# Kernel optimization log

Measured on AMD Instinct MI355X. Metric: run time of the kernel, lower is better.

The kernel has to match this reference:

```python
import jax, jax.numpy as jnp
import numpy as np

B = 16384
LEN_VOCAB = 2048
IPD_VOCAB = 2048
EBDIN = 32


def setup_inputs() -> dict:
    key = jax.random.key(0)
    ks = jax.random.split(key, 11)
    return {
        "x": jax.random.randint(ks[0], (B, 1, 2), 0, LEN_VOCAB, dtype=jnp.int64)
        if jax.config.jax_enable_x64 else jax.random.randint(ks[0], (B, 1, 2), 0, LEN_VOCAB),
        "lenebdLUT": jax.random.normal(ks[1], (LEN_VOCAB, EBDIN), jnp.float32),
        "ipdebdLUT": jax.random.normal(ks[2], (IPD_VOCAB, EBDIN), jnp.float32),
        "S1": jax.random.normal(ks[3], (15, 2, 15), jnp.float32),
        "H1": jax.random.normal(ks[4], (45, 4096), jnp.float32),
        "T1": jax.random.normal(ks[5], (15, 15), jnp.float32),
        "LUT1": jax.random.normal(ks[6], (5, 4096, 32), jnp.float32),
        "S2": jax.random.normal(ks[7], (1, 2, 15), jnp.float32),
        "H2": jax.random.normal(ks[8], (15, 16), jnp.float32),
        "T2": jax.random.normal(ks[9], (1, 15), jnp.float32),
        "LUT2": jax.random.normal(ks[10], (1, 16, 32), jnp.float32),
    }


def _forward(x, lenebdLUT, ipdebdLUT, S1, H1, T1, LUT1, S2, H2, T2, LUT2):
    batch = x.shape[0]
    # embedding lookups, summed: [B,1,32] -> flatten to [B,32] (seq==1)
    e = (lenebdLUT[x[:, :, 0]] + ipdebdLUT[x[:, :, 1]]).reshape(-1, EBDIN)
    ebd = e
    # ---- newMM on first 30 features ----
    a = jnp.einsum('bcd,cdk->bck', e[:, :30].reshape(-1, 15, 2), S1)  # [B,15,15]
    a = a - T1 - 1e-4
    t = jnp.tanh(a)
    a = jax.lax.stop_gradient(jnp.sign(a) - t) + t  # straight-through sign
    a = a.reshape(-1, 5, 45)
    scores1 = jnp.einsum('bcd,dk->bck', a, H1)       # [B,5,4096]
    idx1 = jnp.argmax(scores1, axis=-1)              # [B,5]
    # one_hot(argmax) @ LUT == per-codebook gather
    x1 = LUT1[jnp.arange(5)[None, :], idx1]          # [B,5,32]
    # ---- MM_final on last 2 features ----
    b = jnp.einsum('bcd,cdk->bck', e[:, 30:32].reshape(-1, 1, 2), S2)  # [B,1,15]
    b = b - T2
    b = jnp.where(b == 0, jnp.float32(-1.0), jnp.sign(b))  # x[x==0]=-1; sign(x)
    scores2 = jnp.einsum('bcd,dk->bck', b, H2)       # [B,1,16]
    idx2 = jnp.argmax(scores2, axis=-1)              # [B,1]
    x2 = LUT2[jnp.arange(1)[None, :], idx2]          # [B,1,32]
    x2 = jnp.sum(x2, axis=1).reshape(batch, 1, 32)
    reconstruct = jnp.concatenate([x1, x2], axis=1).sum(axis=1)  # [B,32]
    return reconstruct, ebd


def reference(x, lenebdLUT, ipdebdLUT, S1, H1, T1, LUT1, S2, H2, T2, LUT2):
    return _forward(x, lenebdLUT, ipdebdLUT, S1, H1, T1, LUT1, S2, H2, T2, LUT2)
```

## Files before the change

### kernel.cpp

```cpp
#include <hip/hip_runtime.h>

#define B_TOT 16384
#define NPAIR (B_TOT*5)
#define NPT32 (NPAIR/32)
#define NKG   8
#define KTPG  16
#define KTB   9216

#define PREP_BLKS 288
#define SIGN_BLKS 320
#define EMBD_BLKS 64

typedef __attribute__((ext_vector_type(8))) short bf16x8;
typedef __attribute__((ext_vector_type(16))) float f32x16;

struct alignas(8) us4 { unsigned short x, y, z, w; };

__device__ inline unsigned short f2bf(float f) {
    unsigned u = __builtin_bit_cast(unsigned, f);
    unsigned r = u + 0x7fffu + ((u >> 16) & 1u);
    return (unsigned short)(r >> 16);
}
__device__ inline float bf2f(unsigned short b) {
    unsigned u = ((unsigned)b) << 16;
    return __builtin_bit_cast(float, u);
}
__device__ inline float max3f(float a, float b, float c) {
    return fmaxf(fmaxf(a, b), c);
}

__global__ __launch_bounds__(256) void kfront(
    const int* __restrict__ x,
    const float* __restrict__ lenLUT, const float* __restrict__ ipdLUT,
    const float* __restrict__ S1, const float* __restrict__ H1,
    const float* __restrict__ T1,
    const float* __restrict__ S2, const float* __restrict__ H2,
    const float* __restrict__ T2, const float* __restrict__ LUT2,
    float* __restrict__ out, float* __restrict__ p2vec,
    unsigned short* __restrict__ Abuf, unsigned short* __restrict__ Bbuf) {
    const int bid = blockIdx.x;
    const int tid = threadIdx.x;

    if (bid < PREP_BLKS) {
        int blk = bid * 4 + (tid >> 6);
        int kt = blk / 9, rem = blk - kt*9;
        int s = rem / 3, q = rem - s*3;
        int l = tid & 63;
        int h = l >> 5;
        int row = kt*32 + (l & 31);
        unsigned short o[8];
#pragma unroll
        for (int j = 0; j < 8; ++j) {
            int d = 16*s + 4*h + ((j < 4) ? j : (j + 4));
            float v = (d < 45) ? H1[(size_t)d*4096 + row] : 0.f;
            unsigned short bb = 0;
            for (int qq = 0; qq <= q; ++qq) { bb = f2bf(v); v -= bf2f(bb); }
            o[j] = bb;
        }
        unsigned short* dst = Abuf + (size_t)blk*512 + l*8;
        *(us4*)(dst)     = us4{o[0], o[1], o[2], o[3]};
        *(us4*)(dst + 4) = us4{o[4], o[5], o[6], o[7]};
        return;
    }

    if (bid < PREP_BLKS + SIGN_BLKS) {
        int p = (bid - PREP_BLKS) * 256 + tid;
        int b = p / 5;
        int c = p - b * 5;
        int x0 = x[2*b], x1 = x[2*b+1];
        float e[6];
        const float2* l2 = (const float2*)(lenLUT + (size_t)x0*32 + 6*c);
        const float2* i2 = (const float2*)(ipdLUT + (size_t)x1*32 + 6*c);
#pragma unroll
        for (int t = 0; t < 3; ++t) {
            float2 a = l2[t], d = i2[t];
            e[2*t]   = a.x + d.x;
            e[2*t+1] = a.y + d.y;
        }
        unsigned short sg[48];
#pragma unroll
        for (int t = 0; t < 3; ++t) {
            int c15 = 3*c + t;
#pragma unroll
            for (int k = 0; k < 15; ++k) {
                float a = e[2*t] * S1[(2*c15)*15 + k] + e[2*t+1] * S1[(2*c15+1)*15 + k];
                a = a - T1[c15*15 + k];
                a = a - 1e-4f;
                sg[t*15+k] = (a > 0.f) ? (unsigned short)0x3F80u
                           : ((a < 0.f) ? (unsigned short)0xBF80u : (unsigned short)0);
            }
        }
        sg[45] = 0; sg[46] = 0; sg[47] = 0;
        int P = p >> 5, col = p & 31;
        unsigned short* base = Bbuf + (size_t)P*1536;
#pragma unroll
        for (int s = 0; s < 3; ++s) {
            unsigned short* blk = base + s*512;
            *(us4*)(blk + col*8)          = us4{sg[16*s+0],  sg[16*s+1],  sg[16*s+2],  sg[16*s+3]};
            *(us4*)(blk + col*8 + 4)      = us4{sg[16*s+8],  sg[16*s+9],  sg[16*s+10], sg[16*s+11]};
            *(us4*)(blk + (col+32)*8)     = us4{sg[16*s+4],  sg[16*s+5],  sg[16*s+6],  sg[16*s+7]};
            *(us4*)(blk + (col+32)*8 + 4) = us4{sg[16*s+12], sg[16*s+13], sg[16*s+14], sg[16*s+15]};
        }
        return;
    }

    {
        int b = (bid - PREP_BLKS - SIGN_BLKS) * 256 + tid;
        if (b >= B_TOT) return;
        int x0 = x[2*b], x1 = x[2*b+1];
        const float4* l4 = (const float4*)(lenLUT + (size_t)x0*32);
        const float4* i4 = (const float4*)(ipdLUT + (size_t)x1*32);
        float4* o4 = (float4*)(out + (size_t)B_TOT*32 + (size_t)b*32);
        float e30 = 0.f, e31 = 0.f;
#pragma unroll
        for (int j = 0; j < 8; ++j) {
            float4 a = l4[j], c = i4[j];
            float4 sv; sv.x=a.x+c.x; sv.y=a.y+c.y; sv.z=a.z+c.z; sv.w=a.w+c.w;
            o4[j] = sv;
            if (j == 7) { e30 = sv.z; e31 = sv.w; }
        }
        float sb[15];
#pragma unroll
        for (int k = 0; k < 15; ++k) {
            float bb = e30 * S2[k] + e31 * S2[15 + k];
            bb = bb - T2[k];
            sb[k] = (bb > 0.f) ? 1.f : -1.f;
        }
        float best = -3.4e38f; int bi = 0;
#pragma unroll
        for (int k2 = 0; k2 < 16; ++k2) {
            float sc = 0.f;
#pragma unroll
            for (int d = 0; d < 15; ++d) sc = fmaf(sb[d], H2[d*16 + k2], sc);
            if (sc > best) { best = sc; bi = k2; }
        }
        const float4* lr = (const float4*)(LUT2 + (size_t)bi*32);
        float4* pv = (float4*)(p2vec + (size_t)b*32);
#pragma unroll
        for (int j = 0; j < 8; ++j) pv[j] = lr[j];
    }
}

__global__ __launch_bounds__(256, 3) void k2m(
    const unsigned short* __restrict__ Abuf,
    const unsigned short* __restrict__ Bbuf,
    float* __restrict__ pval, int* __restrict__ pidx) {
    const int bid = blockIdx.x;
    const int kg = bid & 7;
    const int pg = bid >> 3;
    const int tid = threadIdx.x;
    const int w = tid >> 6, l = tid & 63;
    const int pt0 = pg*8 + w*2;

    __shared__ __align__(16) char lds[2][KTB];

    bf16x8 Bf[2][3];
#pragma unroll
    for (int i = 0; i < 2; ++i)
#pragma unroll
        for (int s = 0; s < 3; ++s)
            Bf[i][s] = *(const bf16x8*)(Bbuf + ((size_t)(pt0+i)*3 + s)*512 + l*8);

    float bv16[2][16];
    float V[2] = {-3.4e38f, -3.4e38f};
    int bkt[2] = {0, 0};
#pragma unroll
    for (int i = 0; i < 2; ++i)
#pragma unroll
        for (int r = 0; r < 16; ++r) bv16[i][r] = -3.4e38f;

    const char* Asrc = (const char*)Abuf + (size_t)kg*KTPG*KTB;

#pragma unroll
    for (int r = 0; r < 3; ++r) {
        int idx = tid + r*256;
        if (idx < KTB/16)
            __builtin_amdgcn_global_load_lds(
                (const __attribute__((address_space(1))) unsigned int*)(Asrc + (size_t)idx*16),
                (__attribute__((address_space(3))) unsigned int*)(&lds[0][idx*16]),
                16, 0, 0);
    }
    __syncthreads();

    f32x16 zf;
#pragma unroll
    for (int r = 0; r < 16; ++r) zf[r] = 0.f;

    for (int ktl = 0; ktl < 16; ++ktl) {
        const int cur = ktl & 1;
        if (ktl < 15) {
            const char* src = Asrc + (size_t)(ktl+1)*KTB;
#pragma unroll
            for (int r = 0; r < 3; ++r) {
                int idx = tid + r*256;
                if (idx < KTB/16)
                    __builtin_amdgcn_global_load_lds(
                        (const __attribute__((address_space(1))) unsigned int*)(src + (size_t)idx*16),
                        (__attribute__((address_space(3))) unsigned int*)(&lds[cur^1][idx*16]),
                        16, 0, 0);
            }
        }
        {
            const char* ab = &lds[cur][l*16];
            bf16x8 A[9];
#pragma unroll
            for (int f = 0; f < 9; ++f)
                A[f] = *(const bf16x8*)(ab + f*1024);

            f32x16 acc0, acc1;
            acc0 = __builtin_amdgcn_mfma_f32_32x32x16_bf16(A[0], Bf[0][0], zf, 0, 0, 0);
            acc1 = __builtin_amdgcn_mfma_f32_32x32x16_bf16(A[0], Bf[1][0], zf, 0, 0, 0);
#pragma unroll
            for (int s = 0; s < 3; ++s)
#pragma unroll
                for (int q = 0; q < 3; ++q) {
                    if (s == 0 && q == 0) continue;
                    const int f = s*3 + q;
                    acc0 = __builtin_amdgcn_mfma_f32_32x32x16_bf16(A[f], Bf[0][s], acc0, 0, 0, 0);
                    acc1 = __builtin_amdgcn_mfma_f32_32x32x16_bf16(A[f], Bf[1][s], acc1, 0, 0, 0);
                }
#pragma unroll
            for (int i = 0; i < 2; ++i) {
                const f32x16& a = (i == 0) ? acc0 : acc1;
                float m0 = max3f(a[0],  a[1],  a[2]);
                float m1 = max3f(a[3],  a[4],  a[5]);
                float m2 = max3f(a[6],  a[7],  a[8]);
                float m3 = max3f(a[9],  a[10], a[11]);
                float m4 = max3f(a[12], a[13], a[14]);
                float m5 = max3f(m0, m1, a[15]);
                float m6 = max3f(m2, m3, m4);
                float t  = fmaxf(m5, m6);
                bkt[i] = (t > V[i]) ? ktl : bkt[i];
                V[i] = fmaxf(V[i], t);
#pragma unroll
                for (int r = 0; r < 16; ++r)
                    bv16[i][r] = fmaxf(bv16[i][r], a[r]);
            }
        }
        __syncthreads();
    }

    const int h = l >> 5;
#pragma unroll
    for (int i = 0; i < 2; ++i) {
        int rb = 0;
#pragma unroll
        for (int r = 15; r >= 0; --r)
            rb = (bv16[i][r] == V[i]) ? r : rb;
        int kk = kg*512 + bkt[i]*32 + (rb & 3) + ((rb >> 2) << 3) + (h << 2);
        float v = V[i];
        float ov = __shfl_xor(v, 32);
        int   ok = __shfl_xor(kk, 32);
        if (ov > v || (ov == v && ok < kk)) { v = ov; kk = ok; }
        if (l < 32) {
            int pair = (pt0 + i)*32 + l;
            pval[(size_t)pair*NKG + kg] = v;
            pidx[(size_t)pair*NKG + kg] = kk;
        }
    }
}

__global__ __launch_bounds__(256) void k3_final(
    const float* __restrict__ pval, const int* __restrict__ pidx,
    const float* __restrict__ LUT1, const float* __restrict__ p2vec,
    float* __restrict__ out) {
    int t = blockIdx.x * 256 + threadIdx.x;
    int b = t >> 3, j = t & 7;
    if (b >= B_TOT) return;
    float4 r = ((const float4*)(p2vec + (size_t)b*32))[j];
#pragma unroll
    for (int c = 0; c < 5; ++c) {
        size_t pair = (size_t)b*5 + c;
        const float4* pv4 = (const float4*)(pval + pair*NKG);
        const int4*   pi4 = (const int4*)(pidx + pair*NKG);
        float4 v0 = pv4[0], v1 = pv4[1];
        int4   i0 = pi4[0], i1 = pi4[1];
        float vv[8] = {v0.x, v0.y, v0.z, v0.w, v1.x, v1.y, v1.z, v1.w};
        int   ii[8] = {i0.x, i0.y, i0.z, i0.w, i1.x, i1.y, i1.z, i1.w};
        float bvv = vv[0]; int bk = ii[0];
#pragma unroll
        for (int q = 1; q < 8; ++q) {
            if (vv[q] > bvv) { bvv = vv[q]; bk = ii[q]; }
        }
        float4 tl = ((const float4*)(LUT1 + ((size_t)c*4096 + bk)*32))[j];
        r.x += tl.x; r.y += tl.y; r.z += tl.z; r.w += tl.w;
    }
    ((float4*)(out + (size_t)b*32))[j] = r;
}

extern "C" void kernel_launch(void* const* d_in, const int* in_sizes, int n_in,
                              void* d_out, int out_size, void* d_ws, size_t ws_size,
                              hipStream_t stream) {
    const int*   x      = (const int*)d_in[0];
    const float* lenLUT = (const float*)d_in[1];
    const float* ipdLUT = (const float*)d_in[2];
    const float* S1     = (const float*)d_in[3];
    const float* H1     = (const float*)d_in[4];
    const float* T1     = (const float*)d_in[5];
    const float* LUT1   = (const float*)d_in[6];
    const float* S2     = (const float*)d_in[7];
    const float* H2     = (const float*)d_in[8];
    const float* T2     = (const float*)d_in[9];
    const float* LUT2   = (const float*)d_in[10];
    float* out = (float*)d_out;

    char* ws = (char*)d_ws;
    unsigned short* Abuf = (unsigned short*)ws;
    size_t off = (size_t)1152*1024;
    unsigned short* Bbuf = (unsigned short*)(ws + off);
    off += (size_t)NPT32*1536*2;
    float* p2vec = (float*)(ws + off);
    off += (size_t)B_TOT*32*4;
    float* pval  = (float*)(ws + off);
    off += (size_t)NPAIR*NKG*4;
    int*   pidx  = (int*)(ws + off);

    kfront<<<dim3(PREP_BLKS + SIGN_BLKS + EMBD_BLKS), dim3(256), 0, stream>>>(
        x, lenLUT, ipdLUT, S1, H1, T1, S2, H2, T2, LUT2, out, p2vec, Abuf, Bbuf);
    k2m<<<dim3(NPT32), dim3(256), 0, stream>>>(Abuf, Bbuf, pval, pidx);
    k3_final<<<dim3(B_TOT*8/256), dim3(256), 0, stream>>>(
        pval, pidx, LUT1, p2vec, out);
}
```

Before: 103.0 us.

## Load A tiles directly from global into registers, dropping LDS staging

Removes the double-buffered LDS staging of the A (codebook) tiles in the k2m MFMA kernel. Each lane now reads its A fragments straight from global memory (relying on L2/L1 caching, since all four waves read the same tile) and the per-tile __syncthreads is dropped. Launch bounds go from 3 to 2 blocks per SM, giving more registers, and the K loop is unrolled by 2 so loads can be issued ahead. The risk is more global/L1 traffic and exposed load latency without explicit prefetching.

```diff
diff --git a/kernel.cpp b/kernel.cpp
--- a/kernel.cpp
+++ b/kernel.cpp
@@ -141,7 +141,7 @@
     }
 }
 
-__global__ __launch_bounds__(256, 3) void k2m(
+__global__ __launch_bounds__(256, 2) void k2m(
     const unsigned short* __restrict__ Abuf,
     const unsigned short* __restrict__ Bbuf,
     float* __restrict__ pval, int* __restrict__ pidx) {
@@ -152,8 +152,6 @@
     const int w = tid >> 6, l = tid & 63;
     const int pt0 = pg*8 + w*2;
 
-    __shared__ __align__(16) char lds[2][KTB];
-
     bf16x8 Bf[2][3];
 #pragma unroll
     for (int i = 0; i < 2; ++i)
@@ -169,75 +167,49 @@
 #pragma unroll
         for (int r = 0; r < 16; ++r) bv16[i][r] = -3.4e38f;
 
-    const char* Asrc = (const char*)Abuf + (size_t)kg*KTPG*KTB;
-
-#pragma unroll
-    for (int r = 0; r < 3; ++r) {
-        int idx = tid + r*256;
-        if (idx < KTB/16)
-            __builtin_amdgcn_global_load_lds(
-                (const __attribute__((address_space(1))) unsigned int*)(Asrc + (size_t)idx*16),
-                (__attribute__((address_space(3))) unsigned int*)(&lds[0][idx*16]),
-                16, 0, 0);
-    }
-    __syncthreads();
+    const char* Asrc = (const char*)Abuf + (size_t)kg*KTPG*KTB + (size_t)l*16;
 
     f32x16 zf;
 #pragma unroll
     for (int r = 0; r < 16; ++r) zf[r] = 0.f;
 
+#pragma unroll 2
     for (int ktl = 0; ktl < 16; ++ktl) {
-        const int cur = ktl & 1;
-        if (ktl < 15) {
-            const char* src = Asrc + (size_t)(ktl+1)*KTB;
-#pragma unroll
-            for (int r = 0; r < 3; ++r) {
-                int idx = tid + r*256;
-                if (idx < KTB/16)
-                    __builtin_amdgcn_global_load_lds(
-                        (const __attribute__((address_space(1))) unsigned int*)(src + (size_t)idx*16),
-                        (__attribute__((address_space(3))) unsigned int*)(&lds[cur^1][idx*16]),
-                        16, 0, 0);
+        const char* ab = Asrc + (size_t)ktl*KTB;
+        bf16x8 A[9];
+#pragma unroll
+        for (int f = 0; f < 9; ++f)
+            A[f] = *(const bf16x8*)(ab + f*1024);
+
+        f32x16 acc0, acc1;
+        acc0 = __builtin_amdgcn_mfma_f32_32x32x16_bf16(A[0], Bf[0][0], zf, 0, 0, 0);
+        acc1 = __builtin_amdgcn_mfma_f32_32x32x16_bf16(A[0], Bf[1][0], zf, 0, 0, 0);
+#pragma unroll
+        for (int s = 0; s < 3; ++s)
+#pragma unroll
+            for (int q = 0; q < 3; ++q) {
+                if (s == 0 && q == 0) continue;
+                const int f = s*3 + q;
+                acc0 = __builtin_amdgcn_mfma_f32_32x32x16_bf16(A[f], Bf[0][s], acc0, 0, 0, 0);
+                acc1 = __builtin_amdgcn_mfma_f32_32x32x16_bf16(A[f], Bf[1][s], acc1, 0, 0, 0);
             }
-        }
-        {
-            const char* ab = &lds[cur][l*16];
-            bf16x8 A[9];
-#pragma unroll
-            for (int f = 0; f < 9; ++f)
-                A[f] = *(const bf16x8*)(ab + f*1024);
-
-            f32x16 acc0, acc1;
-            acc0 = __builtin_amdgcn_mfma_f32_32x32x16_bf16(A[0], Bf[0][0], zf, 0, 0, 0);
-            acc1 = __builtin_amdgcn_mfma_f32_32x32x16_bf16(A[0], Bf[1][0], zf, 0, 0, 0);
-#pragma unroll
-            for (int s = 0; s < 3; ++s)
-#pragma unroll
-                for (int q = 0; q < 3; ++q) {
-                    if (s == 0 && q == 0) continue;
-                    const int f = s*3 + q;
-                    acc0 = __builtin_amdgcn_mfma_f32_32x32x16_bf16(A[f], Bf[0][s], acc0, 0, 0, 0);
-                    acc1 = __builtin_amdgcn_mfma_f32_32x32x16_bf16(A[f], Bf[1][s], acc1, 0, 0, 0);
-                }
-#pragma unroll
-            for (int i = 0; i < 2; ++i) {
-                const f32x16& a = (i == 0) ? acc0 : acc1;
-                float m0 = max3f(a[0],  a[1],  a[2]);
-                float m1 = max3f(a[3],  a[4],  a[5]);
-                float m2 = max3f(a[6],  a[7],  a[8]);
-                float m3 = max3f(a[9],  a[10], a[11]);
-                float m4 = max3f(a[12], a[13], a[14]);
-                float m5 = max3f(m0, m1, a[15]);
-                float m6 = max3f(m2, m3, m4);
-                float t  = fmaxf(m5, m6);
-                bkt[i] = (t > V[i]) ? ktl : bkt[i];
-                V[i] = fmaxf(V[i], t);
-#pragma unroll
-                for (int r = 0; r < 16; ++r)
-                    bv16[i][r] = fmaxf(bv16[i][r], a[r]);
-            }
-        }
-        __syncthreads();
+#pragma unroll
+        for (int i = 0; i < 2; ++i) {
+            const f32x16& a = (i == 0) ? acc0 : acc1;
+            float m0 = max3f(a[0],  a[1],  a[2]);
+            float m1 = max3f(a[3],  a[4],  a[5]);
+            float m2 = max3f(a[6],  a[7],  a[8]);
+            float m3 = max3f(a[9],  a[10], a[11]);
+            float m4 = max3f(a[12], a[13], a[14]);
+            float m5 = max3f(m0, m1, a[15]);
+            float m6 = max3f(m2, m3, m4);
+            float t  = fmaxf(m5, m6);
+            bkt[i] = (t > V[i]) ? ktl : bkt[i];
+            V[i] = fmaxf(V[i], t);
+#pragma unroll
+            for (int r = 0; r < 16; ++r)
+                bv16[i][r] = fmaxf(bv16[i][r], a[r]);
+        }
     }
 
     const int h = l >> 5;
```

After: 102.5 us. Within noise of the previous version (-0.6%).
